# Kernel tuning notes

Hardware: AMD Instinct MI355X
Metric: run time of the kernel (lower is better)

## Reference

```python
import jax, jax.numpy as jnp
import numpy as np

NUM_HEADS = 8

def setup_inputs() -> dict:
    key = jax.random.key(0)
    ks = jax.random.split(key, 9)
    b, s, d = 2, 2048, 512
    e = d * NUM_HEADS  # 4096
    sc = 0.02
    return {
        "x": jax.random.normal(ks[0], (b, s, d), jnp.float32),
        "Wq": jax.random.normal(ks[1], (e, d), jnp.float32) * sc,
        "bq": jax.random.normal(ks[2], (e,), jnp.float32) * sc,
        "Wk": jax.random.normal(ks[3], (e, d), jnp.float32) * sc,
        "bk": jax.random.normal(ks[4], (e,), jnp.float32) * sc,
        "Wv": jax.random.normal(ks[5], (e, d), jnp.float32) * sc,
        "bv": jax.random.normal(ks[6], (e,), jnp.float32) * sc,
        "Wo": jax.random.normal(ks[7], (d, e), jnp.float32) * sc,
        "bo": jax.random.normal(ks[8], (d,), jnp.float32) * sc,
    }

def reference(x, Wq, bq, Wk, bk, Wv, bv, Wo, bo):
    b, s, d = x.shape
    h = NUM_HEADS
    hd = d  # head_dim == model_dimension in this module
    # QKV projections: [b, s, h*hd]
    q = (x @ Wq.T + bq).reshape(b, s, h, hd)
    k = (x @ Wk.T + bk).reshape(b, s, h, hd)
    v = (x @ Wv.T + bv).reshape(b, s, h, hd)
    # scores: [b, h, s_q, s_k]
    scores = jnp.einsum("bqhd,bkhd->bhqk", q, k) / jnp.sqrt(jnp.float32(hd))
    attn = jax.nn.softmax(scores, axis=-1)
    ctx = jnp.einsum("bhqk,bkhd->bqhd", attn, v).reshape(b, s, h * hd)
    return ctx @ Wo.T + bo
```

## Files before the change

### kernel.cpp

```cpp
#include <hip/hip_runtime.h>
#include <hip/hip_bf16.h>

typedef __hip_bfloat16 bf16t;
typedef short bf16x8 __attribute__((ext_vector_type(8)));
typedef float f32x4 __attribute__((ext_vector_type(4)));

__device__ __forceinline__ unsigned short f2b(float f) {
    unsigned u;
    __builtin_memcpy(&u, &f, 4);
    unsigned r = (u + 0x7fffu + ((u >> 16) & 1u)) >> 16;
    return (unsigned short)r;
}

__device__ __forceinline__ void gload_lds16(const void* g, void* l) {
    __builtin_amdgcn_global_load_lds(
        (const __attribute__((address_space(1))) void*)g,
        (__attribute__((address_space(3))) void*)l,
        16, 0, 0);
}

template<int EPI>
__global__ __launch_bounds__(512, 2)
void gemm8p(const bf16t* __restrict__ Ag, const bf16t* __restrict__ Bg,
            void* __restrict__ Cg, const float* __restrict__ bias,
            float* __restrict__ part,
            int K, int lda, int ldb, int ldc,
            long aOffB, long aOffH, long bOffB, long bOffH,
            long cOffB, long cOffH, float scale)
{
    __shared__ __align__(16) char lds8[131072];

    unsigned gx = gridDim.x, gy = gridDim.y;
    unsigned nwg = gx * gy * gridDim.z;
    unsigned wg = (blockIdx.z * gy + blockIdx.y) * gx + blockIdx.x;
    if ((nwg & 7u) == 0u) wg = (wg & 7u) * (nwg >> 3) + (wg >> 3);
    const unsigned pz = wg / (gx * gy);
    const unsigned prem = wg - pz * gx * gy;
    const unsigned py = prem / gx;
    const unsigned px = prem - py * gx;

    const int zb = pz >> 3, zh = pz & 7;
    const int brow = py * 256;
    const int bcol = px * 256;

    const size_t ldab = (size_t)lda * 2;
    const size_t ldbb = (size_t)ldb * 2;
    const char* Agb = (const char*)(Ag + (size_t)zb * aOffB + (size_t)zh * aOffH)
                      + (size_t)brow * ldab;
    const char* Bgb = (const char*)(Bg + (size_t)zb * bOffB + (size_t)zh * bOffH)
                      + (size_t)bcol * ldbb;

    const int t    = threadIdx.x;
    const int lane = t & 63;
    const int wid  = t >> 6;
    const int wm   = wid >> 2;
    const int wn   = wid & 3;
    const int lr   = lane & 15;
    const int lk   = lane >> 4;

    const int srow = t >> 2;
    const int scg  = (t & 3) ^ ((srow >> 1) & 3);
    const size_t aSrc = (size_t)srow * ldab + (size_t)scg * 16;
    const size_t bSrc = (size_t)srow * ldbb + (size_t)scg * 16;
    const int dst0 = t * 16;
    char* ldsA = lds8;
    char* ldsB = lds8 + 65536;

    const int rchunk = lk ^ ((lr >> 1) & 3);
    const int aByte = (wm * 128 + lr) * 64 + rchunk * 16;
    const int bByte = (wn * 64 + lr) * 64 + rchunk * 16;

    f32x4 acc[8][4];
#pragma unroll
    for (int i = 0; i < 8; ++i)
#pragma unroll
        for (int j = 0; j < 4; ++j)
            acc[i][j] = (f32x4){0.f, 0.f, 0.f, 0.f};

    const int nk = K >> 5;

#define STAGE_A(kt, bufi) do {                                              \
        const char* s_ = Agb + (size_t)(kt) * 64 + aSrc;                    \
        char* d_ = ldsA + (bufi) * 16384 + dst0;                            \
        gload_lds16(s_, d_);                                                \
        gload_lds16(s_ + 128 * ldab, d_ + 8192);                            \
    } while (0)
#define STAGE_B(kt, bufi) do {                                              \
        const char* s_ = Bgb + (size_t)(kt) * 64 + bSrc;                    \
        char* d_ = ldsB + (bufi) * 16384 + dst0;                            \
        gload_lds16(s_, d_);                                                \
        gload_lds16(s_ + 128 * ldbb, d_ + 8192);                            \
    } while (0)

    const int npro = nk < 3 ? nk : 3;
    for (int p = 0; p < npro; ++p) { STAGE_A(p, p & 3); STAGE_B(p, p & 3); }
    if (npro == 3) asm volatile("s_waitcnt vmcnt(8)" ::: "memory");
    else           asm volatile("s_waitcnt vmcnt(0)" ::: "memory");
    __builtin_amdgcn_s_barrier();

    for (int kt = 0; kt < nk; ++kt) {
        const int buf  = kt & 3;
        const int bufS = (kt + 3) & 3;
        const bool st  = (kt + 3) < nk;
        const char* lA = ldsA + buf * 16384;
        const char* lB = ldsB + buf * 16384;

        bf16x8 af[4], bfv[4];
#pragma unroll
        for (int i = 0; i < 4; ++i) af[i]  = *(const bf16x8*)(lA + aByte + i * 1024);
#pragma unroll
        for (int j = 0; j < 4; ++j) bfv[j] = *(const bf16x8*)(lB + bByte + j * 1024);
        if (st) STAGE_A(kt + 3, bufS);
        __builtin_amdgcn_s_barrier();
        asm volatile("s_waitcnt lgkmcnt(0)" ::: "memory");
        __builtin_amdgcn_s_setprio(1);
#pragma unroll
        for (int i = 0; i < 4; ++i)
#pragma unroll
            for (int j = 0; j < 4; ++j)
                acc[i][j] = __builtin_amdgcn_mfma_f32_16x16x32_bf16(af[i], bfv[j], acc[i][j], 0, 0, 0);
        __builtin_amdgcn_s_setprio(0);
        asm volatile("" ::: "memory");
        __builtin_amdgcn_s_barrier();

        bf16x8 af2[4];
#pragma unroll
        for (int i = 0; i < 4; ++i) af2[i] = *(const bf16x8*)(lA + aByte + (i + 4) * 1024);
        if (st) STAGE_B(kt + 3, bufS);
        if (st)                  asm volatile("s_waitcnt vmcnt(8)" ::: "memory");
        else if (kt + 2 < nk)    asm volatile("s_waitcnt vmcnt(4)" ::: "memory");
        else if (kt + 1 < nk)    asm volatile("s_waitcnt vmcnt(0)" ::: "memory");
        __builtin_amdgcn_s_barrier();
        asm volatile("s_waitcnt lgkmcnt(0)" ::: "memory");
        __builtin_amdgcn_s_setprio(1);
#pragma unroll
        for (int i = 0; i < 4; ++i)
#pragma unroll
            for (int j = 0; j < 4; ++j)
                acc[i + 4][j] = __builtin_amdgcn_mfma_f32_16x16x32_bf16(af2[i], bfv[j], acc[i + 4][j], 0, 0, 0);
        __builtin_amdgcn_s_setprio(0);
        asm volatile("" ::: "memory");
        __builtin_amdgcn_s_barrier();
    }
#undef STAGE_A
#undef STAGE_B

    if (EPI == 4) {
        __syncthreads();
        unsigned short* lC = (unsigned short*)lds8;
#pragma unroll
        for (int i = 0; i < 8; ++i)
#pragma unroll
            for (int j = 0; j < 4; ++j) {
                int col = wn * 64 + j * 16 + lr;
#pragma unroll
                for (int r = 0; r < 4; ++r) {
                    int row = wm * 128 + i * 16 + lk * 4 + r;
                    lC[row * 256 + col] = f2b(__expf(acc[i][j][r] * scale));
                }
            }
        __syncthreads();
        unsigned short* C = (unsigned short*)((bf16t*)Cg + (size_t)zb * cOffB + (size_t)zh * cOffH);
#pragma unroll
        for (int p = 0; p < 16; ++p) {
            int c  = p * 512 + t;
            int row = c >> 5;
            int cc  = c & 31;
            bf16x8 v = *(const bf16x8*)(lC + (size_t)c * 8);
            *(bf16x8*)(C + (size_t)(brow + row) * ldc + bcol + cc * 8) = v;
        }
    } else {
        const int sel = bcol >> 12;
        const int colw0 = bcol & 4095;
        if (sel < 2) {
            __syncthreads();
            unsigned short* lC = (unsigned short*)lds8;
#pragma unroll
            for (int i = 0; i < 8; ++i)
#pragma unroll
                for (int j = 0; j < 4; ++j) {
                    int col = wn * 64 + j * 16 + lr;
                    float badd = bias[bcol + col];
#pragma unroll
                    for (int r = 0; r < 4; ++r) {
                        int row = wm * 128 + i * 16 + lk * 4 + r;
                        lC[row * 256 + col] = f2b(acc[i][j][r] + badd);
                    }
                }
            __syncthreads();
            unsigned short* C = (unsigned short*)((bf16t*)Cg + (size_t)sel * cOffB);
#pragma unroll
            for (int p = 0; p < 16; ++p) {
                int c  = p * 512 + t;
                int row = c >> 5;
                int cc  = c & 31;
                bf16x8 v = *(const bf16x8*)(lC + (size_t)c * 8);
                *(bf16x8*)(C + (size_t)(brow + row) * ldc + colw0 + cc * 8) = v;
            }
        } else {
            unsigned short* C = (unsigned short*)part;
#pragma unroll
            for (int i = 0; i < 8; ++i)
#pragma unroll
                for (int j = 0; j < 4; ++j) {
                    int col = colw0 + wn * 64 + j * 16 + lr;
                    int hh = col >> 9, dd = col & 511;
                    float badd = bias[8192 + col];
                    int row0 = brow + wm * 128 + i * 16 + lk * 4;
                    int bb = row0 >> 11, ss0 = row0 & 2047;
                    ushort4 pack;
                    pack.x = f2b(acc[i][j][0] + badd);
                    pack.y = f2b(acc[i][j][1] + badd);
                    pack.z = f2b(acc[i][j][2] + badd);
                    pack.w = f2b(acc[i][j][3] + badd);
                    size_t addr = ((((size_t)(bb * 8 + hh)) * 512 + dd) << 11) + (size_t)ss0;
                    *(ushort4*)(C + addr) = pack;
                }
        }
    }
}

__global__ __launch_bounds__(512, 1)
void gemm_pv(const bf16t* __restrict__ Eg, const bf16t* __restrict__ Vg,
             bf16t* __restrict__ Cg)
{
    __shared__ __align__(16) char lds[122880];

    unsigned wg = blockIdx.x;
    wg = (wg & 7u) * 32u + (wg >> 3);
    const int pz = wg >> 4;
    const int py = wg & 15;
    const int zb = pz >> 3, zh = pz & 7;
    const int brow = py * 128;

    const char* Agb = (const char*)Eg + ((size_t)pz * 2048 * 2048 + (size_t)brow * 2048) * 2;
    const char* Bgb = (const char*)Vg + ((size_t)pz * 512 * 2048) * 2;

    const int t    = threadIdx.x;
    const int lane = t & 63;
    const int wid  = t >> 6;
    const int wm   = wid >> 2;
    const int wn   = wid & 3;
    const int lr   = lane & 15;
    const int lk   = lane >> 4;

    const int srow = t >> 2;
    const int scg  = (t & 3) ^ ((srow >> 1) & 3);
    const size_t aSrc = (size_t)srow * 4096 + (size_t)scg * 16;
    const size_t bSrc = (size_t)srow * 4096 + (size_t)scg * 16;
    char* ldsA = lds;
    char* ldsB = lds + 24576;

    const int rchunk = lk ^ ((lr >> 1) & 3);
    const int aByte = (wm * 64 + lr) * 64 + rchunk * 16;
    const int bByte = (wn * 128 + lr) * 64 + rchunk * 16;

    f32x4 acc[4][8];
#pragma unroll
    for (int i = 0; i < 4; ++i)
#pragma unroll
        for (int j = 0; j < 8; ++j)
            acc[i][j] = (f32x4){0.f, 0.f, 0.f, 0.f};
    f32x4 accS[4];
#pragma unroll
    for (int i = 0; i < 4; ++i) accS[i] = (f32x4){0.f, 0.f, 0.f, 0.f};

    bf16x8 ones;
#pragma unroll
    for (int e = 0; e < 8; ++e) ones[e] = (short)0x3F80;

#define STAGE_PV(kt, bufi) do {                                             \
        const char* sa_ = Agb + (size_t)(kt) * 64 + aSrc;                   \
        gload_lds16(sa_, ldsA + (bufi) * 8192 + t * 16);                    \
        const char* sb_ = Bgb + (size_t)(kt) * 64 + bSrc;                   \
        char* db_ = ldsB + (bufi) * 32768 + t * 16;                         \
        gload_lds16(sb_,               db_);                                \
        gload_lds16(sb_ + 128 * 4096,  db_ + 8192);                         \
        gload_lds16(sb_ + 256 * 4096,  db_ + 16384);                        \
        gload_lds16(sb_ + 384 * 4096,  db_ + 24576);                        \
    } while (0)

    const int nk = 64;
    STAGE_PV(0, 0);
    STAGE_PV(1, 1);
    asm volatile("s_waitcnt vmcnt(5)" ::: "memory");
    __builtin_amdgcn_s_barrier();

    int bufR = 0, bufS = 2;
    for (int kt = 0; kt < nk; ++kt) {
        const char* lA = ldsA + bufR * 8192;
        const char* lB = ldsB + bufR * 32768;

        bf16x8 af[4], bfv[8];
#pragma unroll
        for (int i = 0; i < 4; ++i) af[i]  = *(const bf16x8*)(lA + aByte + i * 1024);
#pragma unroll
        for (int j = 0; j < 8; ++j) bfv[j] = *(const bf16x8*)(lB + bByte + j * 1024);

        if (kt + 2 < nk) {
            STAGE_PV(kt + 2, bufS);
            asm volatile("s_waitcnt vmcnt(5)" ::: "memory");
        } else if (kt + 1 < nk) {
            asm volatile("s_waitcnt vmcnt(0)" ::: "memory");
        }
        __builtin_amdgcn_s_barrier();
        asm volatile("s_waitcnt lgkmcnt(0)" ::: "memory");
        __builtin_amdgcn_s_setprio(1);
#pragma unroll
        for (int i = 0; i < 4; ++i) {
            accS[i] = __builtin_amdgcn_mfma_f32_16x16x32_bf16(af[i], ones, accS[i], 0, 0, 0);
#pragma unroll
            for (int j = 0; j < 8; ++j)
                acc[i][j] = __builtin_amdgcn_mfma_f32_16x16x32_bf16(af[i], bfv[j], acc[i][j], 0, 0, 0);
        }
        __builtin_amdgcn_s_setprio(0);
        asm volatile("" ::: "memory");
        __builtin_amdgcn_s_barrier();

        bufR = (bufR == 2) ? 0 : bufR + 1;
        bufS = (bufS == 2) ? 0 : bufS + 1;
    }
#undef STAGE_PV

    float inv_[4][4];
#pragma unroll
    for (int i = 0; i < 4; ++i)
#pragma unroll
        for (int r = 0; r < 4; ++r)
            inv_[i][r] = 1.0f / accS[i][r];

    unsigned short* lC = (unsigned short*)lds;
    unsigned short* C = (unsigned short*)(Cg + (size_t)zb * 2048 * 4096 + (size_t)zh * 512);
#pragma unroll
    for (int m = 0; m < 2; ++m) {
        __syncthreads();
        if (wm == m) {
#pragma unroll
            for (int i = 0; i < 4; ++i)
#pragma unroll
                for (int j = 0; j < 8; ++j) {
                    int col = wn * 128 + j * 16 + lr;
#pragma unroll
                    for (int r = 0; r < 4; ++r) {
                        int row = i * 16 + lk * 4 + r;
                        lC[row * 512 + col] = f2b(acc[i][j][r] * inv_[i][r]);
                    }
                }
        }
        __syncthreads();
#pragma unroll
        for (int p = 0; p < 8; ++p) {
            int c  = p * 512 + t;
            int row = c >> 6;
            int cc  = c & 63;
            bf16x8 v = *(const bf16x8*)(lC + (size_t)c * 8);
            *(bf16x8*)(C + (size_t)(brow + m * 64 + row) * 4096 + cc * 8) = v;
        }
    }
}

__global__ __launch_bounds__(256, 3)
void gemm_of32(const bf16t* __restrict__ Ag, const bf16t* __restrict__ Bg,
               float* __restrict__ Cg, const float* __restrict__ bias,
               int K, int lda, int ldb, int ldc)
{
    __shared__ __align__(16) char lds[49152];

    unsigned gx = gridDim.x, gy = gridDim.y;
    unsigned nwg = gx * gy;
    unsigned wg = blockIdx.y * gx + blockIdx.x;
    if ((nwg & 7u) == 0u) wg = (wg & 7u) * (nwg >> 3) + (wg >> 3);
    const unsigned py = wg / gx;
    const unsigned px = wg - py * gx;
    const int brow = py * 128;
    const int bcol = px * 64;

    const int t    = threadIdx.x;
    const int lane = t & 63;
    const int wid  = t >> 6;
    const int wr   = wid >> 1, wc = wid & 1;
    const int lr   = lane & 15;
    const int lk   = lane >> 4;

    const size_t ldab = (size_t)lda * 2;
    const size_t ldbb = (size_t)ldb * 2;
    const char* Agb = (const char*)Ag + (size_t)brow * ldab;
    const char* Bgb = (const char*)Bg + (size_t)bcol * ldbb;

    const int srow = t >> 2;
    const int scg  = (t & 3) ^ ((srow >> 1) & 3);
    const size_t aSrc = (size_t)srow * ldab + (size_t)scg * 16;
    const size_t bSrc = (size_t)srow * ldbb + (size_t)scg * 16;
    char* ldsA = lds;
    char* ldsB = lds + 32768;

    const int rchunk = lk ^ ((lr >> 1) & 3);
    const int aByte = (wr * 64 + lr) * 64 + rchunk * 16;
    const int bByte = (wc * 32 + lr) * 64 + rchunk * 16;

    f32x4 acc[4][2];
#pragma unroll
    for (int i = 0; i < 4; ++i)
#pragma unroll
        for (int j = 0; j < 2; ++j)
            acc[i][j] = (f32x4){0.f, 0.f, 0.f, 0.f};

    const int nk = K >> 5;

#define STAGE_O(kt, bufi) do {                                              \
        const char* sa_ = Agb + (size_t)(kt) * 64 + aSrc;                   \
        gload_lds16(sa_,             ldsA + (bufi) * 8192 + t * 16);        \
        gload_lds16(sa_ + 64 * ldab, ldsA + (bufi) * 8192 + 4096 + t * 16); \
        gload_lds16(Bgb + (size_t)(kt) * 64 + bSrc,                         \
                    ldsB + (bufi) * 4096 + t * 16);                         \
    } while (0)

    for (int p = 0; p < 3; ++p) STAGE_O(p, p);
    asm volatile("s_waitcnt vmcnt(6)" ::: "memory");
    __builtin_amdgcn_s_barrier();

    for (int kt = 0; kt < nk; ++kt) {
        const int buf  = kt & 3;
        const bool st  = (kt + 3) < nk;
        const char* lA = ldsA + buf * 8192;
        const char* lB = ldsB + buf * 4096;

        bf16x8 af[4], bfv[2];
#pragma unroll
        for (int i = 0; i < 4; ++i) af[i]  = *(const bf16x8*)(lA + aByte + i * 1024);
#pragma unroll
        for (int j = 0; j < 2; ++j) bfv[j] = *(const bf16x8*)(lB + bByte + j * 1024);
        if (st) STAGE_O(kt + 3, (kt + 3) & 3);
        if (st)                  asm volatile("s_waitcnt vmcnt(6)" ::: "memory");
        else if (kt + 2 < nk)    asm volatile("s_waitcnt vmcnt(3)" ::: "memory");
        else if (kt + 1 < nk)    asm volatile("s_waitcnt vmcnt(0)" ::: "memory");
        __builtin_amdgcn_s_barrier();
        asm volatile("s_waitcnt lgkmcnt(0)" ::: "memory");
        __builtin_amdgcn_s_setprio(1);
#pragma unroll
        for (int i = 0; i < 4; ++i)
#pragma unroll
            for (int j = 0; j < 2; ++j)
                acc[i][j] = __builtin_amdgcn_mfma_f32_16x16x32_bf16(af[i], bfv[j], acc[i][j], 0, 0, 0);
        __builtin_amdgcn_s_setprio(0);
        asm volatile("" ::: "memory");
        __builtin_amdgcn_s_barrier();
    }
#undef STAGE_O

    const int orow = brow + wr * 64;
    const int ocol = bcol + wc * 32;
#pragma unroll
    for (int i = 0; i < 4; ++i)
#pragma unroll
        for (int j = 0; j < 2; ++j) {
            int col = ocol + j * 16 + lr;
            float badd = bias[col];
#pragma unroll
            for (int r = 0; r < 4; ++r) {
                int row = orow + i * 16 + lk * 4 + r;
                Cg[(size_t)row * ldc + col] = acc[i][j][r] + badd;
            }
        }
}

__global__ __launch_bounds__(256)
void cvt6(const float* __restrict__ s0, const float* __restrict__ s1,
          const float* __restrict__ s2, const float* __restrict__ s3,
          const float* __restrict__ s4,
          bf16t* __restrict__ d0, bf16t* __restrict__ d1,
          bf16t* __restrict__ d2, bf16t* __restrict__ d3,
          bf16t* __restrict__ d4,
          const float* __restrict__ bq, const float* __restrict__ bk,
          const float* __restrict__ bv, float* __restrict__ bqkv)
{
    int i = blockIdx.x * 256 + threadIdx.x;
    if (blockIdx.y == 5) {
        if (i < 3072) {
            int e = i * 4;
            const float* src = (e < 4096) ? (bq + e) : (e < 8192) ? (bk + e - 4096) : (bv + e - 8192);
            float4 f = *(const float4*)src;
            *(float4*)(bqkv + e) = f;
        }
        return;
    }
    const float* s;
    bf16t* d;
    switch (blockIdx.y) {
        case 0: s = s0; d = d0; break;
        case 1: s = s1; d = d1; break;
        case 2: s = s2; d = d2; break;
        case 3: s = s3; d = d3; break;
        default: s = s4; d = d4; break;
    }
    float4 f = ((const float4*)s)[i];
    ushort4 o;
    o.x = f2b(f.x); o.y = f2b(f.y); o.z = f2b(f.z); o.w = f2b(f.w);
    ((ushort4*)d)[i] = o;
}

extern "C" void kernel_launch(void* const* d_in, const int* in_sizes, int n_in,
                              void* d_out, int out_size, void* d_ws, size_t ws_size,
                              hipStream_t stream)
{
    const float* x  = (const float*)d_in[0];
    const float* Wq = (const float*)d_in[1];
    const float* bq = (const float*)d_in[2];
    const float* Wk = (const float*)d_in[3];
    const float* bk = (const float*)d_in[4];
    const float* Wv = (const float*)d_in[5];
    const float* bv = (const float*)d_in[6];
    const float* Wo = (const float*)d_in[7];
    const float* bo = (const float*)d_in[8];

    const int Bn = 2, Sn = 2048, Dn = 512, Hn = 8, En = 4096;
    const int Mn = Bn * Sn;
    const float scl = 0.044194173824159216f;

    bf16t* base = (bf16t*)d_ws;
    size_t off = 0;
    bf16t* Qb  = base + off; off += (size_t)Mn * En;
    bf16t* Kb  = base + off; off += (size_t)Mn * En;
    bf16t* Vt  = base + off; off += (size_t)Mn * En;
    bf16t* Xb  = base + off; off += (size_t)Mn * Dn;
    bf16t* Wc  = base + off; off += (size_t)3 * En * Dn;
    bf16t* Wob = base + off; off += (size_t)Dn * En;
    float* Pbias = (float*)(base + off); off += 12288;
    bf16t* Sb  = base + off;

    cvt6<<<dim3(2048, 6, 1), 256, 0, stream>>>(
        x, Wq, Wk, Wv, Wo,
        Xb, Wc, Wc + (size_t)En * Dn, Wc + (size_t)2 * En * Dn, Wob,
        bq, bk, bv, Pbias);

    gemm8p<5><<<dim3(3 * En / 256, Mn / 256, 1), 512, 0, stream>>>(
        Xb, Wc, Qb, Pbias, (float*)Vt, Dn, Dn, Dn, En,
        0, 0, 0, 0, (long)Mn * En, 0, 1.0f);

    gemm8p<4><<<dim3(Sn / 256, Sn / 256, 16), 512, 0, stream>>>(
        Qb, Kb, Sb, nullptr, nullptr, Dn, En, En, Sn,
        (long)Sn * En, (long)Dn, (long)Sn * En, (long)Dn,
        (long)Hn * Sn * Sn, (long)Sn * Sn, scl);

    gemm_pv<<<256, 512, 0, stream>>>(Sb, Vt, Qb);

    gemm_of32<<<dim3(Dn / 64, Mn / 128, 1), 256, 0, stream>>>(
        Qb, Wob, (float*)d_out, bo, En, En, En, Dn);
}
```

Measured before the change: 299.9 us.

## Fuse score GEMM, exp and PV GEMM into one attention kernel

Replaces the templated batched QK^T GEMM and the separate PV GEMM with one kernel per (batch-head, 128-row query tile). The kernel computes the exponentiated scores tile by tile and writes them to a per-block global scratch area. It accumulates the fp32 row sums in registers instead of using an extra ones-MFMA, then runs the PV GEMM over that scratch. This removes one kernel launch and the separate row-sum MFMAs. In exchange the score phase runs as 256 blocks at one block per CU instead of many smaller tiles, which lowers parallelism, and the exp scores still make a round trip through global memory.

```diff
diff --git a/kernel.cpp b/kernel.cpp
--- a/kernel.cpp
+++ b/kernel.cpp
@@ -19,36 +19,26 @@
         16, 0, 0);
 }
 
-template<int EPI>
 __global__ __launch_bounds__(512, 2)
-void gemm8p(const bf16t* __restrict__ Ag, const bf16t* __restrict__ Bg,
-            void* __restrict__ Cg, const float* __restrict__ bias,
-            float* __restrict__ part,
-            int K, int lda, int ldb, int ldc,
-            long aOffB, long aOffH, long bOffB, long bOffH,
-            long cOffB, long cOffH, float scale)
+void gemm_qkv(const bf16t* __restrict__ Ag, const bf16t* __restrict__ Bg,
+              bf16t* __restrict__ Cg, const float* __restrict__ bias,
+              bf16t* __restrict__ VtB, long cOffB)
 {
     __shared__ __align__(16) char lds8[131072];
 
     unsigned gx = gridDim.x, gy = gridDim.y;
-    unsigned nwg = gx * gy * gridDim.z;
-    unsigned wg = (blockIdx.z * gy + blockIdx.y) * gx + blockIdx.x;
+    unsigned nwg = gx * gy;
+    unsigned wg = blockIdx.y * gx + blockIdx.x;
     if ((nwg & 7u) == 0u) wg = (wg & 7u) * (nwg >> 3) + (wg >> 3);
-    const unsigned pz = wg / (gx * gy);
-    const unsigned prem = wg - pz * gx * gy;
-    const unsigned py = prem / gx;
-    const unsigned px = prem - py * gx;
-
-    const int zb = pz >> 3, zh = pz & 7;
+    const unsigned py = wg / gx;
+    const unsigned px = wg - py * gx;
     const int brow = py * 256;
     const int bcol = px * 256;
 
-    const size_t ldab = (size_t)lda * 2;
-    const size_t ldbb = (size_t)ldb * 2;
-    const char* Agb = (const char*)(Ag + (size_t)zb * aOffB + (size_t)zh * aOffH)
-                      + (size_t)brow * ldab;
-    const char* Bgb = (const char*)(Bg + (size_t)zb * bOffB + (size_t)zh * bOffH)
-                      + (size_t)bcol * ldbb;
+    const size_t ldab = 1024;
+    const size_t ldbb = 1024;
+    const char* Agb = (const char*)Ag + (size_t)brow * ldab;
+    const char* Bgb = (const char*)Bg + (size_t)bcol * ldbb;
 
     const int t    = threadIdx.x;
     const int lane = t & 63;
@@ -77,7 +67,7 @@
         for (int j = 0; j < 4; ++j)
             acc[i][j] = (f32x4){0.f, 0.f, 0.f, 0.f};
 
-    const int nk = K >> 5;
+    const int nk = 16;
 
 #define STAGE_A(kt, bufi) do {                                              \
         const char* s_ = Agb + (size_t)(kt) * 64 + aSrc;                    \
@@ -92,10 +82,8 @@
         gload_lds16(s_ + 128 * ldbb, d_ + 8192);                            \
     } while (0)
 
-    const int npro = nk < 3 ? nk : 3;
-    for (int p = 0; p < npro; ++p) { STAGE_A(p, p & 3); STAGE_B(p, p & 3); }
-    if (npro == 3) asm volatile("s_waitcnt vmcnt(8)" ::: "memory");
-    else           asm volatile("s_waitcnt vmcnt(0)" ::: "memory");
+    for (int p = 0; p < 3; ++p) { STAGE_A(p, p & 3); STAGE_B(p, p & 3); }
+    asm volatile("s_waitcnt vmcnt(8)" ::: "memory");
     __builtin_amdgcn_s_barrier();
 
     for (int kt = 0; kt < nk; ++kt) {
@@ -145,7 +133,9 @@
 #undef STAGE_A
 #undef STAGE_B
 
-    if (EPI == 4) {
+    const int sel = bcol >> 12;
+    const int colw0 = bcol & 4095;
+    if (sel < 2) {
         __syncthreads();
         unsigned short* lC = (unsigned short*)lds8;
 #pragma unroll
@@ -153,88 +143,56 @@
 #pragma unroll
             for (int j = 0; j < 4; ++j) {
                 int col = wn * 64 + j * 16 + lr;
+                float badd = bias[bcol + col];
 #pragma unroll
                 for (int r = 0; r < 4; ++r) {
                     int row = wm * 128 + i * 16 + lk * 4 + r;
-                    lC[row * 256 + col] = f2b(__expf(acc[i][j][r] * scale));
+                    lC[row * 256 + col] = f2b(acc[i][j][r] + badd);
                 }
             }
         __syncthreads();
-        unsigned short* C = (unsigned short*)((bf16t*)Cg + (size_t)zb * cOffB + (size_t)zh * cOffH);
+        unsigned short* C = (unsigned short*)(Cg + (size_t)sel * cOffB);
 #pragma unroll
         for (int p = 0; p < 16; ++p) {
             int c  = p * 512 + t;
             int row = c >> 5;
             int cc  = c & 31;
             bf16x8 v = *(const bf16x8*)(lC + (size_t)c * 8);
-            *(bf16x8*)(C + (size_t)(brow + row) * ldc + bcol + cc * 8) = v;
+            *(bf16x8*)(C + (size_t)(brow + row) * 4096 + colw0 + cc * 8) = v;
         }
     } else {
-        const int sel = bcol >> 12;
-        const int colw0 = bcol & 4095;
-        if (sel < 2) {
-            __syncthreads();
-            unsigned short* lC = (unsigned short*)lds8;
-#pragma unroll
-            for (int i = 0; i < 8; ++i)
-#pragma unroll
-                for (int j = 0; j < 4; ++j) {
-                    int col = wn * 64 + j * 16 + lr;
-                    float badd = bias[bcol + col];
-#pragma unroll
-                    for (int r = 0; r < 4; ++r) {
-                        int row = wm * 128 + i * 16 + lk * 4 + r;
-                        lC[row * 256 + col] = f2b(acc[i][j][r] + badd);
-                    }
-                }
-            __syncthreads();
-            unsigned short* C = (unsigned short*)((bf16t*)Cg + (size_t)sel * cOffB);
-#pragma unroll
-            for (int p = 0; p < 16; ++p) {
-                int c  = p * 512 + t;
-                int row = c >> 5;
-                int cc  = c & 31;
-                bf16x8 v = *(const bf16x8*)(lC + (size_t)c * 8);
-                *(bf16x8*)(C + (size_t)(brow + row) * ldc + colw0 + cc * 8) = v;
+        unsigned short* C = (unsigned short*)VtB;
+#pragma unroll
+        for (int i = 0; i < 8; ++i)
+#pragma unroll
+            for (int j = 0; j < 4; ++j) {
+                int col = colw0 + wn * 64 + j * 16 + lr;
+                int hh = col >> 9, dd = col & 511;
+                float badd = bias[8192 + col];
+                int row0 = brow + wm * 128 + i * 16 + lk * 4;
+                int bb = row0 >> 11, ss0 = row0 & 2047;
+                ushort4 pack;
+                pack.x = f2b(acc[i][j][0] + badd);
+                pack.y = f2b(acc[i][j][1] + badd);
+                pack.z = f2b(acc[i][j][2] + badd);
+                pack.w = f2b(acc[i][j][3] + badd);
+                size_t addr = ((((size_t)(bb * 8 + hh)) * 512 + dd) << 11) + (size_t)ss0;
+                *(ushort4*)(C + addr) = pack;
             }
-        } else {
-            unsigned short* C = (unsigned short*)part;
-#pragma unroll
-            for (int i = 0; i < 8; ++i)
-#pragma unroll
-                for (int j = 0; j < 4; ++j) {
-                    int col = colw0 + wn * 64 + j * 16 + lr;
-                    int hh = col >> 9, dd = col & 511;
-                    float badd = bias[8192 + col];
-                    int row0 = brow + wm * 128 + i * 16 + lk * 4;
-                    int bb = row0 >> 11, ss0 = row0 & 2047;
-                    ushort4 pack;
-                    pack.x = f2b(acc[i][j][0] + badd);
-                    pack.y = f2b(acc[i][j][1] + badd);
-                    pack.z = f2b(acc[i][j][2] + badd);
-                    pack.w = f2b(acc[i][j][3] + badd);
-                    size_t addr = ((((size_t)(bb * 8 + hh)) * 512 + dd) << 11) + (size_t)ss0;
-                    *(ushort4*)(C + addr) = pack;
-                }
-        }
     }
 }
 
 __global__ __launch_bounds__(512, 1)
-void gemm_pv(const bf16t* __restrict__ Eg, const bf16t* __restrict__ Vg,
-             bf16t* __restrict__ Cg)
+void attn_fused(const bf16t* __restrict__ Qg, const bf16t* __restrict__ Kg,
+                const bf16t* __restrict__ Vtg, bf16t* __restrict__ Esc,
+                bf16t* __restrict__ Cg, float scale)
 {
-    __shared__ __align__(16) char lds[122880];
-
-    unsigned wg = blockIdx.x;
-    wg = (wg & 7u) * 32u + (wg >> 3);
-    const int pz = wg >> 4;
-    const int py = wg & 15;
-    const int zb = pz >> 3, zh = pz & 7;
-    const int brow = py * 128;
-
-    const char* Agb = (const char*)Eg + ((size_t)pz * 2048 * 2048 + (size_t)brow * 2048) * 2;
-    const char* Bgb = (const char*)Vg + ((size_t)pz * 512 * 2048) * 2;
+    __shared__ __align__(16) char lds[131072];
+
+    unsigned bid = blockIdx.x;
+    unsigned swz = (bid & 7u) * 32u + (bid >> 3);
+    const int z  = swz >> 4, qt = swz & 15;
+    const int zb = z >> 3, zh = z & 7;
 
     const int t    = threadIdx.x;
     const int lane = t & 63;
@@ -244,16 +202,20 @@
     const int lr   = lane & 15;
     const int lk   = lane >> 4;
 
+    const size_t ldq = 8192;
+    const char* Agb = (const char*)Qg + ((size_t)(zb * 2048 + qt * 128) * 4096 + (size_t)zh * 512) * 2;
+    const char* Bgb = (const char*)Kg + ((size_t)(zb * 2048) * 4096 + (size_t)zh * 512) * 2;
+    unsigned short* Eb = (unsigned short*)(Esc + (size_t)swz * 128 * 2048);
+
     const int srow = t >> 2;
     const int scg  = (t & 3) ^ ((srow >> 1) & 3);
-    const size_t aSrc = (size_t)srow * 4096 + (size_t)scg * 16;
-    const size_t bSrc = (size_t)srow * 4096 + (size_t)scg * 16;
+    const size_t aSrc = (size_t)srow * ldq + (size_t)scg * 16;
+    const size_t bSrc = (size_t)srow * ldq + (size_t)scg * 16;
     char* ldsA = lds;
-    char* ldsB = lds + 24576;
-
+    char* ldsB = lds + 32768;
     const int rchunk = lk ^ ((lr >> 1) & 3);
     const int aByte = (wm * 64 + lr) * 64 + rchunk * 16;
-    const int bByte = (wn * 128 + lr) * 64 + rchunk * 16;
+    const int bByte = (wn * 64 + lr) * 64 + rchunk * 16;
 
     f32x4 acc[4][8];
 #pragma unroll
@@ -261,58 +223,200 @@
 #pragma unroll
         for (int j = 0; j < 8; ++j)
             acc[i][j] = (f32x4){0.f, 0.f, 0.f, 0.f};
-    f32x4 accS[4];
-#pragma unroll
-    for (int i = 0; i < 4; ++i) accS[i] = (f32x4){0.f, 0.f, 0.f, 0.f};
-
-    bf16x8 ones;
-#pragma unroll
-    for (int e = 0; e < 8; ++e) ones[e] = (short)0x3F80;
-
-#define STAGE_PV(kt, bufi) do {                                             \
-        const char* sa_ = Agb + (size_t)(kt) * 64 + aSrc;                   \
-        gload_lds16(sa_, ldsA + (bufi) * 8192 + t * 16);                    \
-        const char* sb_ = Bgb + (size_t)(kt) * 64 + bSrc;                   \
-        char* db_ = ldsB + (bufi) * 32768 + t * 16;                         \
-        gload_lds16(sb_,               db_);                                \
-        gload_lds16(sb_ + 128 * 4096,  db_ + 8192);                         \
-        gload_lds16(sb_ + 256 * 4096,  db_ + 16384);                        \
-        gload_lds16(sb_ + 384 * 4096,  db_ + 24576);                        \
+    float rs[4][4];
+#pragma unroll
+    for (int i = 0; i < 4; ++i)
+#pragma unroll
+        for (int r = 0; r < 4; ++r)
+            rs[i][r] = 0.f;
+
+#define STG_AB(g, bufi) do {                                                \
+        gload_lds16(Agb + (size_t)((g) & 15) * 64 + aSrc,                   \
+                    ldsA + (bufi) * 8192 + t * 16);                         \
+        const char* sb_ = Bgb + (size_t)((g) >> 4) * 256 * ldq              \
+                          + (size_t)((g) & 15) * 64 + bSrc;                 \
+        char* db_ = ldsB + (bufi) * 16384 + t * 16;                         \
+        gload_lds16(sb_, db_);                                              \
+        gload_lds16(sb_ + 128 * ldq, db_ + 8192);                           \
     } while (0)
 
-    const int nk = 64;
-    STAGE_PV(0, 0);
-    STAGE_PV(1, 1);
+    STG_AB(0, 0); STG_AB(1, 1); STG_AB(2, 2);
+    asm volatile("s_waitcnt vmcnt(6)" ::: "memory");
+    __builtin_amdgcn_s_barrier();
+
+    for (int g = 0; g < 128; ++g) {
+        const int buf = g & 3;
+        const char* lA = ldsA + buf * 8192;
+        const char* lB = ldsB + buf * 16384;
+
+        bf16x8 af[4], bfv[4];
+#pragma unroll
+        for (int i = 0; i < 4; ++i) af[i]  = *(const bf16x8*)(lA + aByte + i * 1024);
+#pragma unroll
+        for (int j = 0; j < 4; ++j) bfv[j] = *(const bf16x8*)(lB + bByte + j * 1024);
+
+        if (g + 3 < 128) {
+            STG_AB(g + 3, (g + 3) & 3);
+            asm volatile("s_waitcnt vmcnt(6)" ::: "memory");
+        } else if (g + 2 < 128) {
+            asm volatile("s_waitcnt vmcnt(3)" ::: "memory");
+        } else if (g + 1 < 128) {
+            asm volatile("s_waitcnt vmcnt(0)" ::: "memory");
+        }
+        __builtin_amdgcn_s_barrier();
+        asm volatile("s_waitcnt lgkmcnt(0)" ::: "memory");
+        __builtin_amdgcn_s_setprio(1);
+#pragma unroll
+        for (int i = 0; i < 4; ++i)
+#pragma unroll
+            for (int j = 0; j < 4; ++j)
+                acc[i][j] = __builtin_amdgcn_mfma_f32_16x16x32_bf16(af[i], bfv[j], acc[i][j], 0, 0, 0);
+        __builtin_amdgcn_s_setprio(0);
+        asm volatile("" ::: "memory");
+        __builtin_amdgcn_s_barrier();
+
+        if ((g & 15) == 15) {
+            const int nt = g >> 4;
+#pragma unroll
+            for (int i = 0; i < 4; ++i)
+#pragma unroll
+                for (int j = 0; j < 4; ++j)
+#pragma unroll
+                    for (int r = 0; r < 4; ++r)
+                        acc[i][j][r] = __expf(acc[i][j][r] * scale);
+#pragma unroll
+            for (int i = 0; i < 4; ++i)
+#pragma unroll
+                for (int r = 0; r < 4; ++r)
+                    rs[i][r] += acc[i][0][r] + acc[i][1][r] + acc[i][2][r] + acc[i][3][r];
+
+            unsigned short* epi = (unsigned short*)(lds + 98304);
+#pragma unroll
+            for (int m = 0; m < 2; ++m) {
+                if (wm == m) {
+#pragma unroll
+                    for (int i = 0; i < 4; ++i)
+#pragma unroll
+                        for (int j = 0; j < 4; ++j) {
+                            int col = wn * 64 + j * 16 + lr;
+#pragma unroll
+                            for (int r = 0; r < 4; ++r)
+                                epi[(i * 16 + lk * 4 + r) * 256 + col] = f2b(acc[i][j][r]);
+                        }
+                }
+                asm volatile("s_waitcnt lgkmcnt(0)" ::: "memory");
+                __builtin_amdgcn_s_barrier();
+#pragma unroll
+                for (int p = 0; p < 4; ++p) {
+                    int c  = p * 512 + t;
+                    int row = c >> 5;
+                    int cc  = c & 31;
+                    bf16x8 v = *(const bf16x8*)(epi + (size_t)c * 8);
+                    *(bf16x8*)(Eb + (size_t)(m * 64 + row) * 2048 + nt * 256 + cc * 8) = v;
+                }
+                asm volatile("s_waitcnt lgkmcnt(0)" ::: "memory");
+                __builtin_amdgcn_s_barrier();
+            }
+#pragma unroll
+            for (int i = 0; i < 4; ++i)
+#pragma unroll
+                for (int j = 0; j < 4; ++j)
+                    acc[i][j] = (f32x4){0.f, 0.f, 0.f, 0.f};
+        }
+    }
+#undef STG_AB
+
+    asm volatile("s_waitcnt vmcnt(0) lgkmcnt(0)" ::: "memory");
+    __builtin_amdgcn_s_barrier();
+
+#pragma unroll
+    for (int i = 0; i < 4; ++i)
+#pragma unroll
+        for (int r = 0; r < 4; ++r) {
+            float v = rs[i][r];
+            v += __shfl_xor(v, 1);
+            v += __shfl_xor(v, 2);
+            v += __shfl_xor(v, 4);
+            v += __shfl_xor(v, 8);
+            rs[i][r] = v;
+        }
+    float* tbl = (float*)(lds + 98304);
+    if (lr == 0) {
+#pragma unroll
+        for (int i = 0; i < 4; ++i)
+#pragma unroll
+            for (int r = 0; r < 4; ++r)
+                tbl[(wm * 64 + i * 16 + lk * 4 + r) * 4 + wn] = rs[i][r];
+    }
+    asm volatile("s_waitcnt lgkmcnt(0)" ::: "memory");
+    __builtin_amdgcn_s_barrier();
+    float inv_[4][4];
+#pragma unroll
+    for (int i = 0; i < 4; ++i)
+#pragma unroll
+        for (int r = 0; r < 4; ++r) {
+            int row = wm * 64 + i * 16 + lk * 4 + r;
+            float4 v4 = *(const float4*)(tbl + row * 4);
+            inv_[i][r] = 1.0f / (v4.x + v4.y + v4.z + v4.w);
+        }
+    asm volatile("s_waitcnt lgkmcnt(0)" ::: "memory");
+    __builtin_amdgcn_s_barrier();
+
+    const char* A2 = (const char*)Eb;
+    const char* B2 = (const char*)Vtg + (size_t)z * 512 * 2048 * 2;
+    char* ldsA2 = lds;
+    char* ldsB2 = lds + 24576;
+    const size_t a2Src = (size_t)srow * 4096 + (size_t)scg * 16;
+    const size_t b2Src = (size_t)srow * 4096 + (size_t)scg * 16;
+    const int bByte2 = (wn * 128 + lr) * 64 + rchunk * 16;
+
+#pragma unroll
+    for (int i = 0; i < 4; ++i)
+#pragma unroll
+        for (int j = 0; j < 8; ++j)
+            acc[i][j] = (f32x4){0.f, 0.f, 0.f, 0.f};
+
+#define STG_PV(kt, bufi) do {                                               \
+        gload_lds16(A2 + (size_t)(kt) * 64 + a2Src,                         \
+                    ldsA2 + (bufi) * 8192 + t * 16);                        \
+        const char* sb_ = B2 + (size_t)(kt) * 64 + b2Src;                   \
+        char* db_ = ldsB2 + (bufi) * 32768 + t * 16;                        \
+        gload_lds16(sb_,              db_);                                 \
+        gload_lds16(sb_ + 128 * 4096, db_ + 8192);                          \
+        gload_lds16(sb_ + 256 * 4096, db_ + 16384);                         \
+        gload_lds16(sb_ + 384 * 4096, db_ + 24576);                         \
+    } while (0)
+
+    STG_PV(0, 0);
+    STG_PV(1, 1);
     asm volatile("s_waitcnt vmcnt(5)" ::: "memory");
     __builtin_amdgcn_s_barrier();
 
     int bufR = 0, bufS = 2;
-    for (int kt = 0; kt < nk; ++kt) {
-        const char* lA = ldsA + bufR * 8192;
-        const char* lB = ldsB + bufR * 32768;
+    for (int kt = 0; kt < 64; ++kt) {
+        const char* lA = ldsA2 + bufR * 8192;
+        const char* lB = ldsB2 + bufR * 32768;
 
         bf16x8 af[4], bfv[8];
 #pragma unroll
         for (int i = 0; i < 4; ++i) af[i]  = *(const bf16x8*)(lA + aByte + i * 1024);
 #pragma unroll
-        for (int j = 0; j < 8; ++j) bfv[j] = *(const bf16x8*)(lB + bByte + j * 1024);
-
-        if (kt + 2 < nk) {
-            STAGE_PV(kt + 2, bufS);
+        for (int j = 0; j < 8; ++j) bfv[j] = *(const bf16x8*)(lB + bByte2 + j * 1024);
+
+        if (kt + 2 < 64) {
+            STG_PV(kt + 2, bufS);
             asm volatile("s_waitcnt vmcnt(5)" ::: "memory");
-        } else if (kt + 1 < nk) {
+        } else if (kt + 1 < 64) {
             asm volatile("s_waitcnt vmcnt(0)" ::: "memory");
         }
         __builtin_amdgcn_s_barrier();
         asm volatile("s_waitcnt lgkmcnt(0)" ::: "memory");
         __builtin_amdgcn_s_setprio(1);
 #pragma unroll
-        for (int i = 0; i < 4; ++i) {
-            accS[i] = __builtin_amdgcn_mfma_f32_16x16x32_bf16(af[i], ones, accS[i], 0, 0, 0);
+        for (int i = 0; i < 4; ++i)
 #pragma unroll
             for (int j = 0; j < 8; ++j)
                 acc[i][j] = __builtin_amdgcn_mfma_f32_16x16x32_bf16(af[i], bfv[j], acc[i][j], 0, 0, 0);
-        }
         __builtin_amdgcn_s_setprio(0);
         asm volatile("" ::: "memory");
         __builtin_amdgcn_s_barrier();
@@ -320,17 +424,10 @@
         bufR = (bufR == 2) ? 0 : bufR + 1;
         bufS = (bufS == 2) ? 0 : bufS + 1;
     }
-#undef STAGE_PV
-
-    float inv_[4][4];
-#pragma unroll
-    for (int i = 0; i < 4; ++i)
-#pragma unroll
-        for (int r = 0; r < 4; ++r)
-            inv_[i][r] = 1.0f / accS[i][r];
+#undef STG_PV
 
     unsigned short* lC = (unsigned short*)lds;
-    unsigned short* C = (unsigned short*)(Cg + (size_t)zb * 2048 * 4096 + (size_t)zh * 512);
+    unsigned short* C = (unsigned short*)Cg + (size_t)zb * 2048 * 4096 + (size_t)zh * 512;
 #pragma unroll
     for (int m = 0; m < 2; ++m) {
         __syncthreads();
@@ -354,7 +451,7 @@
             int row = c >> 6;
             int cc  = c & 63;
             bf16x8 v = *(const bf16x8*)(lC + (size_t)c * 8);
-            *(bf16x8*)(C + (size_t)(brow + m * 64 + row) * 4096 + cc * 8) = v;
+            *(bf16x8*)(C + (size_t)(qt * 128 + m * 64 + row) * 4096 + cc * 8) = v;
         }
     }
 }
@@ -513,8 +610,8 @@
     const float* Wo = (const float*)d_in[7];
     const float* bo = (const float*)d_in[8];
 
-    const int Bn = 2, Sn = 2048, Dn = 512, Hn = 8, En = 4096;
-    const int Mn = Bn * Sn;
+    const int Sn = 2048, Dn = 512, En = 4096;
+    const int Mn = 4096;
     const float scl = 0.044194173824159216f;
 
     bf16t* base = (bf16t*)d_ws;
@@ -533,16 +630,10 @@
         Xb, Wc, Wc + (size_t)En * Dn, Wc + (size_t)2 * En * Dn, Wob,
         bq, bk, bv, Pbias);
 
-    gemm8p<5><<<dim3(3 * En / 256, Mn / 256, 1), 512, 0, stream>>>(
-        Xb, Wc, Qb, Pbias, (float*)Vt, Dn, Dn, Dn, En,
-        0, 0, 0, 0, (long)Mn * En, 0, 1.0f);
-
-    gemm8p<4><<<dim3(Sn / 256, Sn / 256, 16), 512, 0, stream>>>(
-        Qb, Kb, Sb, nullptr, nullptr, Dn, En, En, Sn,
-        (long)Sn * En, (long)Dn, (long)Sn * En, (long)Dn,
-        (long)Hn * Sn * Sn, (long)Sn * Sn, scl);
-
-    gemm_pv<<<256, 512, 0, stream>>>(Sb, Vt, Qb);
+    gemm_qkv<<<dim3(3 * En / 256, Mn / 256, 1), 512, 0, stream>>>(
+        Xb, Wc, Qb, Pbias, Vt, (long)Mn * En);
+
+    attn_fused<<<256, 512, 0, stream>>>(Qb, Kb, Vt, Sb, Qb, scl);
 
     gemm_of32<<<dim3(Dn / 64, Mn / 128, 1), 256, 0, stream>>>(
         Qb, Wob, (float*)d_out, bo, En, En, En, Dn);
```

Result: faster. 293.7 us (-2.0%).
